# Kernel optimization log

Hardware: AMD Instinct MI355X
Metric: run time of the kernel (lower is better)

## Reference

```python
import jax, jax.numpy as jnp
import numpy as np

B, M, D, K = 64, 2_000_000, 32, 10
EPS = 1e-5            # kernel epsilon in _inverse_kernel
DENOM_C = 1e-5        # denominator_constant in _episodic_reward


def setup_inputs() -> dict:
    key = jax.random.key(0)
    kq, km = jax.random.split(key)
    query = jax.random.normal(kq, (B, D), dtype=jnp.float32)
    memory = jax.random.normal(km, (M, D), dtype=jnp.float32)
    return {"query": query, "memory": memory, "k": K}


def reference(query, memory, k):
    # Squared Euclidean distances [B, M] via the expanded form (no [B,M,D] intermediate).
    q2 = jnp.sum(query * query, axis=-1, keepdims=True)          # [B, 1]
    m2 = jnp.sum(memory * memory, axis=-1)                       # [M]
    sq = jnp.maximum(q2 + m2[None, :] - 2.0 * (query @ memory.T), 0.0)  # [B, M]
    # Running mean of squared distances (vectorized fixed point of RunningMean;
    # stateful numpy update in the original -> no gradient through it).
    mean_sq = jax.lax.stop_gradient(jnp.mean(sq))
    # _inverse_kernel: eps / (d^2 / mean + eps)
    kdist = EPS / (sq / mean_sq + EPS)                           # [B, M]
    # sklearn kneighbors picks the k SMALLEST metric values.
    neg_topk, _ = jax.lax.top_k(-kdist, k)                       # [B, k]
    neighbor_sum = -jnp.sum(neg_topk, axis=-1)                   # [B]
    # episodic reward: 1 / sqrt(sum(neighbor kernel distances) + c)
    return 1.0 / jnp.sqrt(neighbor_sum + DENOM_C)
```

## Files before the change

### kernel.cpp

```cpp
#include <hip/hip_runtime.h>
#include <hip/hip_bf16.h>
#include <float.h>
#include <math.h>

typedef short short8 __attribute__((ext_vector_type(8)));
typedef float f32x4  __attribute__((ext_vector_type(4)));

#define KEPS   1e-5f
#define DENOMC 1e-5f

__device__ __forceinline__ short f2bf(float x) {
    return __builtin_bit_cast(short, __float2bfloat16(x));
}

__device__ __forceinline__ void gload_lds16(const void* g, void* l) {
    __builtin_amdgcn_global_load_lds(
        (const __attribute__((address_space(1))) void*)g,
        (__attribute__((address_space(3))) void*)l,
        16, 0, 0);
}

__device__ __forceinline__ void top10_insert(float (&lst)[10], float s) {
    if (s > lst[0]) {
        lst[0] = s;
        #pragma unroll
        for (int i = 1; i < 10; ++i) {
            float lo = fminf(lst[0], lst[i]);
            float hi = fmaxf(lst[0], lst[i]);
            lst[0] = lo; lst[i] = hi;
        }
    }
}

__global__ __launch_bounds__(256, 5) void ep_main(
    const float* __restrict__ q, const float* __restrict__ mem,
    float* __restrict__ part_top,
    float* __restrict__ part_sums,
    int nb, int ntiles)
{
    __shared__ __align__(16) char smemc[32768];

    const int tid  = threadIdx.x;
    const int lane = tid & 63;
    const int wave = tid >> 6;
    const int g    = lane >> 4;
    const int c    = lane & 15;
    const int bid  = blockIdx.x;

    const int tpb = ntiles / nb;
    const int rem = ntiles % nb;
    const int t0  = bid * tpb + (bid < rem ? bid : rem);
    const int cnt = tpb + (bid < rem ? 1 : 0);

    short8 qfrag[4];
    #pragma unroll
    for (int h = 0; h < 4; ++h) {
        const float* qp = q + (h * 16 + c) * 32 + g * 8;
        f32x4 w0 = *(const f32x4*)qp;
        f32x4 w1 = *(const f32x4*)(qp + 4);
        short8 f;
        f[0]=f2bf(-2.f*w0[0]); f[1]=f2bf(-2.f*w0[1]); f[2]=f2bf(-2.f*w0[2]); f[3]=f2bf(-2.f*w0[3]);
        f[4]=f2bf(-2.f*w1[0]); f[5]=f2bf(-2.f*w1[1]); f[6]=f2bf(-2.f*w1[2]); f[7]=f2bf(-2.f*w1[3]);
        qfrag[h] = f;
    }

    float t1[16];
    #pragma unroll
    for (int i = 0; i < 16; ++i) t1[i] = -FLT_MAX;
    float cs[8];
    #pragma unroll
    for (int r = 0; r < 8; ++r) cs[r] = 0.f;
    float sumsq = 0.f;

    char* ring = smemc + wave * 8192;
    const int    sw    = ((lane >> 3) & 3) << 1;
    const size_t so    = (size_t)((lane ^ sw) * 16);
    const size_t rdoff = (size_t)(((c * 8 + g * 2) ^ ((c & 3) << 1)) * 16);

    auto process = [&](const char* buf) {
        const f32x4* rp = (const f32x4*)(buf + rdoff);
        f32x4 v0 = rp[0];
        f32x4 v1 = rp[1];

        float ps;
        ps = v0[0] * v0[0];
        ps = fmaf(v0[1], v0[1], ps);
        ps = fmaf(v0[2], v0[2], ps);
        ps = fmaf(v0[3], v0[3], ps);
        ps = fmaf(v1[0], v1[0], ps);
        ps = fmaf(v1[1], v1[1], ps);
        ps = fmaf(v1[2], v1[2], ps);
        ps = fmaf(v1[3], v1[3], ps);
        sumsq += ps;
        cs[0] += v0[0]; cs[1] += v0[1]; cs[2] += v0[2]; cs[3] += v0[3];
        cs[4] += v1[0]; cs[5] += v1[1]; cs[6] += v1[2]; cs[7] += v1[3];

        float m2 = ps + __shfl_xor(ps, 16, 64);
        m2 = m2 + __shfl_xor(m2, 32, 64);
        f32x4 mi = {m2, m2, m2, m2};

        short8 mf;
        mf[0]=f2bf(v0[0]); mf[1]=f2bf(v0[1]); mf[2]=f2bf(v0[2]); mf[3]=f2bf(v0[3]);
        mf[4]=f2bf(v1[0]); mf[5]=f2bf(v1[1]); mf[6]=f2bf(v1[2]); mf[7]=f2bf(v1[3]);

        #pragma unroll
        for (int h = 0; h < 4; ++h) {
            f32x4 acc = __builtin_amdgcn_mfma_f32_16x16x32_bf16(qfrag[h], mf, mi, 0, 0, 0);
            t1[h*4+0] = fmaxf(t1[h*4+0], acc[0]);
            t1[h*4+1] = fmaxf(t1[h*4+1], acc[1]);
            t1[h*4+2] = fmaxf(t1[h*4+2], acc[2]);
            t1[h*4+3] = fmaxf(t1[h*4+3], acc[3]);
        }
    };

    const char* gstage = (const char*)mem + (size_t)t0 * 8192 + (size_t)wave * 2048 + so;

    const int nst = cnt < 3 ? cnt : 3;
    for (int d = 0; d < nst; ++d) {
        char* dst = ring + (d & 3) * 2048;
        gload_lds16(gstage,        dst);
        gload_lds16(gstage + 1024, dst + 1024);
        gstage += 8192;
    }
    for (int i = 0; i + 3 < cnt; ++i) {
        char* dst = ring + ((i + 3) & 3) * 2048;
        gload_lds16(gstage,        dst);
        gload_lds16(gstage + 1024, dst + 1024);
        gstage += 8192;
        asm volatile("s_waitcnt vmcnt(6)" ::: "memory");
        process(ring + (i & 3) * 2048);
    }
    if (cnt >= 3) {
        asm volatile("s_waitcnt vmcnt(4)" ::: "memory");
        process(ring + ((cnt - 3) & 3) * 2048);
    }
    if (cnt >= 2) {
        asm volatile("s_waitcnt vmcnt(2)" ::: "memory");
        process(ring + ((cnt - 2) & 3) * 2048);
    }
    asm volatile("s_waitcnt vmcnt(0)" ::: "memory");
    process(ring + ((cnt - 1) & 3) * 2048);

    __syncthreads();
    float (*ltop)[65] = (float (*)[65])smemc;
    float (*red)[4][8] = (float (*)[4][8])(smemc + 16640);
    float* ssred = (float*)(smemc + 17152);

    const int col = wave * 16 + c;
    #pragma unroll
    for (int h = 0; h < 4; ++h) {
        #pragma unroll
        for (int r = 0; r < 4; ++r)
            ltop[h * 16 + g * 4 + r][col] = t1[h * 4 + r];
    }

    #pragma unroll
    for (int r = 0; r < 8; ++r) {
        float v = cs[r];
        v += __shfl_xor(v, 1, 64);
        v += __shfl_xor(v, 2, 64);
        v += __shfl_xor(v, 4, 64);
        v += __shfl_xor(v, 8, 64);
        cs[r] = v;
    }
    float ssv = sumsq;
    ssv += __shfl_xor(ssv, 1, 64);
    ssv += __shfl_xor(ssv, 2, 64);
    ssv += __shfl_xor(ssv, 4, 64);
    ssv += __shfl_xor(ssv, 8, 64);
    ssv += __shfl_xor(ssv, 16, 64);
    ssv += __shfl_xor(ssv, 32, 64);
    if (c == 0) {
        #pragma unroll
        for (int r = 0; r < 8; ++r) red[wave][g][r] = cs[r];
    }
    if (lane == 0) ssred[wave] = ssv;
    __syncthreads();

    if (tid < 32) {
        float a = red[0][tid >> 3][tid & 7] + red[1][tid >> 3][tid & 7]
                + red[2][tid >> 3][tid & 7] + red[3][tid >> 3][tid & 7];
        part_sums[(size_t)tid * nb + bid] = a;
    } else if (tid == 32) {
        part_sums[(size_t)32 * nb + bid] = ssred[0] + ssred[1] + ssred[2] + ssred[3];
    }

    if (tid < 64) {
        float lst[10];
        #pragma unroll
        for (int i = 0; i < 10; ++i) lst[i] = -FLT_MAX;
        #pragma unroll 4
        for (int s2 = 0; s2 < 64; ++s2) top10_insert(lst, ltop[tid][s2]);
        #pragma unroll
        for (int i = 0; i < 10; ++i)
            part_top[((size_t)tid * nb + bid) * 10 + i] = lst[i];
    }
}

__global__ __launch_bounds__(256) void ep_tail(
    const float* __restrict__ q, const float* __restrict__ part_top,
    const float* __restrict__ part_sums, float* __restrict__ out,
    int nb, int Mrows)
{
    const int b    = blockIdx.x;
    const int tid  = threadIdx.x;
    const int lane = tid & 63;
    const int wave = tid >> 6;

    __shared__ float smem[256 * 33];
    __shared__ float colsum_a[33];
    __shared__ float w4[4];
    __shared__ float mean_s, q2_s;

    if (tid < 64) {
        float x = (tid < 32) ? q[b * 32 + tid] : 0.f;
        float a = x * x;
        a += __shfl_xor(a, 1, 64);
        a += __shfl_xor(a, 2, 64);
        a += __shfl_xor(a, 4, 64);
        a += __shfl_xor(a, 8, 64);
        a += __shfl_xor(a, 16, 64);
        if (tid == 0) q2_s = a;
    }

    float a2 = 0.f;
    #pragma unroll
    for (int e = 0; e < 8; ++e) {
        float x = q[tid * 8 + e];
        a2 = fmaf(x, x, a2);
    }
    a2 += __shfl_xor(a2, 1, 64);
    a2 += __shfl_xor(a2, 2, 64);
    a2 += __shfl_xor(a2, 4, 64);
    a2 += __shfl_xor(a2, 8, 64);
    a2 += __shfl_xor(a2, 16, 64);
    a2 += __shfl_xor(a2, 32, 64);
    if (lane == 0) w4[wave] = a2;

    float acc[33];
    #pragma unroll
    for (int c2 = 0; c2 < 33; ++c2) acc[c2] = 0.f;
    for (int i = tid; i < nb; i += 256) {
        #pragma unroll
        for (int c2 = 0; c2 < 33; ++c2) acc[c2] += part_sums[(size_t)c2 * nb + i];
    }
    #pragma unroll
    for (int c2 = 0; c2 < 33; ++c2) smem[tid * 33 + c2] = acc[c2];
    __syncthreads();
    if (tid < 33) {
        float a = 0.f;
        #pragma unroll 16
        for (int j = 0; j < 256; ++j) a += smem[j * 33 + tid];
        colsum_a[tid] = a;
    }
    __syncthreads();

    if (tid < 32) {
        float qs = 0.f;
        #pragma unroll 8
        for (int bb = 0; bb < 64; ++bb) qs += q[bb * 32 + tid];
        float dq = qs * colsum_a[tid];
        dq += __shfl_xor(dq, 1, 64);
        dq += __shfl_xor(dq, 2, 64);
        dq += __shfl_xor(dq, 4, 64);
        dq += __shfl_xor(dq, 8, 64);
        dq += __shfl_xor(dq, 16, 64);
        if (tid == 0) {
            double q2sum = (double)w4[0] + (double)w4[1] + (double)w4[2] + (double)w4[3];
            double sumsq = (double)colsum_a[32];
            double Md    = (double)Mrows;
            mean_s = (float)((Md * q2sum + 64.0 * sumsq - 2.0 * (double)dq) / (64.0 * Md));
        }
    }
    __syncthreads();

    float lst[10];
    #pragma unroll
    for (int i = 0; i < 10; ++i) lst[i] = -FLT_MAX;
    const float* pt = part_top + (size_t)b * nb * 10;
    for (int i = tid; i < nb; i += 256) {
        const float* pp = pt + (size_t)i * 10;
        #pragma unroll
        for (int r = 0; r < 10; ++r) top10_insert(lst, pp[r]);
    }
    #pragma unroll
    for (int r = 0; r < 10; ++r) smem[tid * 10 + r] = lst[r];
    __syncthreads();

    if (tid < 32) {
        float m[10];
        #pragma unroll
        for (int i = 0; i < 10; ++i) m[i] = -FLT_MAX;
        for (int j2 = 0; j2 < 8; ++j2) {
            #pragma unroll
            for (int r = 0; r < 10; ++r) top10_insert(m, smem[(tid * 8 + j2) * 10 + r]);
        }
        #pragma unroll
        for (int r = 0; r < 10; ++r) smem[2560 + tid * 10 + r] = m[r];
    }
    __syncthreads();

    if (tid == 0) {
        float m[10];
        #pragma unroll
        for (int i = 0; i < 10; ++i) m[i] = -FLT_MAX;
        for (int j2 = 0; j2 < 32; ++j2) {
            #pragma unroll
            for (int r = 0; r < 10; ++r) top10_insert(m, smem[2560 + j2 * 10 + r]);
        }
        const float mean = mean_s;
        const float q2b  = q2_s;
        float sum = 0.f;
        #pragma unroll
        for (int r = 0; r < 10; ++r) {
            float sq = m[r] + q2b;
            sq = fmaxf(sq, 0.f);
            sum += KEPS / (sq / mean + KEPS);
        }
        out[b] = 1.0f / sqrtf(sum + DENOMC);
    }
}

extern "C" void kernel_launch(void* const* d_in, const int* in_sizes, int n_in,
                              void* d_out, int out_size, void* d_ws, size_t ws_size,
                              hipStream_t stream)
{
    const float* q   = (const float*)d_in[0];
    const float* mem = (const float*)d_in[1];
    float* out = (float*)d_out;

    const int Mrows  = in_sizes[1] / 32;
    const int ntiles = Mrows / 64;

    int nb = 1280;
    while (nb > 64 && ((size_t)nb * 673 + 64) * sizeof(float) > ws_size) nb >>= 1;
    if (nb > ntiles) nb = ntiles;

    float* part_top  = (float*)d_ws;
    float* part_sums = part_top + (size_t)64 * nb * 10;

    ep_main<<<dim3(nb), dim3(256), 0, stream>>>(q, mem, part_top, part_sums, nb, ntiles);
    ep_tail<<<dim3(64), dim3(256), 0, stream>>>(q, part_top, part_sums, out, nb, Mrows);
}
```

Baseline: 96.52 us.

## Shrink LDS ring to double buffer, raise occupancy and grid size

Replaces the four-deep per-wave LDS ring with a two-slot double buffer, which halves shared memory to about 17KB so more blocks fit per CU. Launch bounds go from 5 to 8 blocks per SM and the grid grows from 1280 to 2048 blocks. The MFMA now accumulates into zero and the m2 norm is added afterwards, so the shuffle reduction can start earlier. The trade is less prefetch depth per wave, with more resident waves expected to hide memory latency, plus tighter register limits.

Measured after the change: 101.8 us. +5.5%, slower.

```diff
diff --git a/kernel.cpp b/kernel.cpp
--- a/kernel.cpp
+++ b/kernel.cpp
@@ -32,13 +32,13 @@
     }
 }
 
-__global__ __launch_bounds__(256, 5) void ep_main(
+__global__ __launch_bounds__(256, 8) void ep_main(
     const float* __restrict__ q, const float* __restrict__ mem,
     float* __restrict__ part_top,
     float* __restrict__ part_sums,
     int nb, int ntiles)
 {
-    __shared__ __align__(16) char smemc[32768];
+    __shared__ __align__(16) char smemc[17408];
 
     const int tid  = threadIdx.x;
     const int lane = tid & 63;
@@ -72,7 +72,7 @@
     for (int r = 0; r < 8; ++r) cs[r] = 0.f;
     float sumsq = 0.f;
 
-    char* ring = smemc + wave * 8192;
+    char* ring = smemc + wave * 4096;
     const int    sw    = ((lane >> 3) & 3) << 1;
     const size_t so    = (size_t)((lane ^ sw) * 16);
     const size_t rdoff = (size_t)(((c * 8 + g * 2) ^ ((c & 3) << 1)) * 16);
@@ -91,60 +91,52 @@
         ps = fmaf(v1[1], v1[1], ps);
         ps = fmaf(v1[2], v1[2], ps);
         ps = fmaf(v1[3], v1[3], ps);
+        float m2 = ps + __shfl_xor(ps, 16, 64);
+        m2 = m2 + __shfl_xor(m2, 32, 64);
+
         sumsq += ps;
         cs[0] += v0[0]; cs[1] += v0[1]; cs[2] += v0[2]; cs[3] += v0[3];
         cs[4] += v1[0]; cs[5] += v1[1]; cs[6] += v1[2]; cs[7] += v1[3];
 
-        float m2 = ps + __shfl_xor(ps, 16, 64);
-        m2 = m2 + __shfl_xor(m2, 32, 64);
-        f32x4 mi = {m2, m2, m2, m2};
-
         short8 mf;
         mf[0]=f2bf(v0[0]); mf[1]=f2bf(v0[1]); mf[2]=f2bf(v0[2]); mf[3]=f2bf(v0[3]);
         mf[4]=f2bf(v1[0]); mf[5]=f2bf(v1[1]); mf[6]=f2bf(v1[2]); mf[7]=f2bf(v1[3]);
 
+        const f32x4 zero = {0.f, 0.f, 0.f, 0.f};
         #pragma unroll
         for (int h = 0; h < 4; ++h) {
-            f32x4 acc = __builtin_amdgcn_mfma_f32_16x16x32_bf16(qfrag[h], mf, mi, 0, 0, 0);
-            t1[h*4+0] = fmaxf(t1[h*4+0], acc[0]);
-            t1[h*4+1] = fmaxf(t1[h*4+1], acc[1]);
-            t1[h*4+2] = fmaxf(t1[h*4+2], acc[2]);
-            t1[h*4+3] = fmaxf(t1[h*4+3], acc[3]);
+            f32x4 acc = __builtin_amdgcn_mfma_f32_16x16x32_bf16(qfrag[h], mf, zero, 0, 0, 0);
+            t1[h*4+0] = fmaxf(t1[h*4+0], acc[0] + m2);
+            t1[h*4+1] = fmaxf(t1[h*4+1], acc[1] + m2);
+            t1[h*4+2] = fmaxf(t1[h*4+2], acc[2] + m2);
+            t1[h*4+3] = fmaxf(t1[h*4+3], acc[3] + m2);
         }
     };
 
-    const char* gstage = (const char*)mem + (size_t)t0 * 8192 + (size_t)wave * 2048 + so;
-
-    const int nst = cnt < 3 ? cnt : 3;
-    for (int d = 0; d < nst; ++d) {
-        char* dst = ring + (d & 3) * 2048;
-        gload_lds16(gstage,        dst);
-        gload_lds16(gstage + 1024, dst + 1024);
-        gstage += 8192;
-    }
-    for (int i = 0; i + 3 < cnt; ++i) {
-        char* dst = ring + ((i + 3) & 3) * 2048;
-        gload_lds16(gstage,        dst);
-        gload_lds16(gstage + 1024, dst + 1024);
-        gstage += 8192;
-        asm volatile("s_waitcnt vmcnt(6)" ::: "memory");
-        process(ring + (i & 3) * 2048);
-    }
-    if (cnt >= 3) {
-        asm volatile("s_waitcnt vmcnt(4)" ::: "memory");
-        process(ring + ((cnt - 3) & 3) * 2048);
-    }
-    if (cnt >= 2) {
-        asm volatile("s_waitcnt vmcnt(2)" ::: "memory");
-        process(ring + ((cnt - 2) & 3) * 2048);
-    }
-    asm volatile("s_waitcnt vmcnt(0)" ::: "memory");
-    process(ring + ((cnt - 1) & 3) * 2048);
-
-    __syncthreads();
-    float (*ltop)[65] = (float (*)[65])smemc;
+    const char* gsrc = (const char*)mem + (size_t)t0 * 8192 + (size_t)wave * 2048 + so;
+
+    gload_lds16(gsrc,        ring);
+    gload_lds16(gsrc + 1024, ring + 1024);
+    gsrc += 8192;
+
+    for (int i = 0; i < cnt; ++i) {
+        const bool more = (i + 1) < cnt;
+        if (more) {
+            char* dst = ring + ((i + 1) & 1) * 2048;
+            gload_lds16(gsrc,        dst);
+            gload_lds16(gsrc + 1024, dst + 1024);
+            gsrc += 8192;
+            asm volatile("s_waitcnt vmcnt(2)" ::: "memory");
+        } else {
+            asm volatile("s_waitcnt vmcnt(0)" ::: "memory");
+        }
+        process(ring + (i & 1) * 2048);
+    }
+
+    __syncthreads();
+    float (*ltop)[65]  = (float (*)[65])smemc;
     float (*red)[4][8] = (float (*)[4][8])(smemc + 16640);
-    float* ssred = (float*)(smemc + 17152);
+    float* ssred       = (float*)(smemc + 17152);
 
     const int col = wave * 16 + c;
     #pragma unroll
@@ -332,7 +324,7 @@
     const int Mrows  = in_sizes[1] / 32;
     const int ntiles = Mrows / 64;
 
-    int nb = 1280;
+    int nb = 2048;
     while (nb > 64 && ((size_t)nb * 673 + 64) * sizeof(float) > ws_size) nb >>= 1;
     if (nb > ntiles) nb = ntiles;
 
```
